# Kernel tuning notes

Hardware: AMD Instinct MI355X
Metric: run time of the kernel (lower is better)

## Reference

```python
import jax, jax.numpy as jnp
import numpy as np

N = 50000      # nodes
E = 800000     # edges (before self-loops)
DIN = 2        # dim_input
DEMB = 128     # dim_embedding
H = 8          # n_heads
DV = 16        # dim_values (H*DV == DEMB)
DH = 512       # dim_hidden
L = 2          # n_att_layers
K = 10         # APPNP steps
ALPHA = 0.1
EPS = 1e-5     # BatchNorm eps
NEG_SLOPE = 0.2  # GAT leaky_relu slope


def setup_inputs() -> dict:
    key = jax.random.key(0)
    ks = jax.random.split(key, 16)
    s = 0.05
    inp = {}
    inp["x"] = jax.random.normal(ks[0], (N, DIN), jnp.float32)
    inp["J"] = jax.random.uniform(ks[1], (N, 1), jnp.float32)
    inp["edge_index"] = jax.random.randint(ks[2], (2, E), 0, N, jnp.int32)
    # Lin1: Linear(dim_input+1, dim_embedding)
    inp["lin0_w"] = jax.random.normal(ks[3], (DIN + 1, DEMB), jnp.float32) * s
    inp["lin0_b"] = jnp.zeros((DEMB,), jnp.float32)
    # Per attention layer (stacked over L):
    inp["gat_w"]   = jax.random.normal(ks[4], (L, DEMB, H * DV), jnp.float32) * s
    inp["att_src"] = jax.random.normal(ks[5], (L, H, DV), jnp.float32) * s
    inp["att_dst"] = jax.random.normal(ks[6], (L, H, DV), jnp.float32) * s
    inp["lin1_w"]  = jax.random.normal(ks[7], (L, DV, DEMB), jnp.float32) * s
    inp["bn1_g"]   = jnp.ones((L, DEMB), jnp.float32)
    inp["bn1_b"]   = jnp.zeros((L, DEMB), jnp.float32)
    inp["lin2_w"]  = jax.random.normal(ks[8], (L, DEMB, DH), jnp.float32) * s
    inp["lin2_b"]  = jnp.zeros((L, DH), jnp.float32)
    inp["lin3_w"]  = jax.random.normal(ks[9], (L, DH, DEMB), jnp.float32) * s
    inp["lin3_b"]  = jnp.zeros((L, DEMB), jnp.float32)
    inp["bn2_g"]   = jnp.ones((L, DEMB), jnp.float32)
    inp["bn2_b"]   = jnp.zeros((L, DEMB), jnp.float32)
    return inp


def _bn(z, g, b):
    # BatchNorm1d over nodes, training-mode batch statistics (biased var)
    mu = z.mean(0)
    var = jnp.mean((z - mu) ** 2, axis=0)
    return g * (z - mu) * jax.lax.rsqrt(var + EPS) + b


def reference(x, J, edge_index, lin0_w, lin0_b, gat_w, att_src, att_dst,
              lin1_w, bn1_g, bn1_b, lin2_w, lin2_b, lin3_w, lin3_b,
              bn2_g, bn2_b):
    # add self-loops (PyG GATConv and APPNP defaults)
    loop = jnp.arange(N, dtype=edge_index.dtype)
    src = jnp.concatenate([edge_index[0], loop])  # message source j
    dst = jnp.concatenate([edge_index[1], loop])  # message target i

    h = jnp.concatenate([x, J], axis=1) @ lin0_w + lin0_b  # [N, DEMB]

    for l in range(L):
        # ---- GATConv ----
        xl = (h @ gat_w[l]).reshape(N, H, DV)                # [N,H,DV]
        a_s = (xl * att_src[l]).sum(-1)                      # [N,H]
        a_d = (xl * att_dst[l]).sum(-1)                      # [N,H]
        e = jax.nn.leaky_relu(a_s[src] + a_d[dst], NEG_SLOPE)  # [E',H]
        e = e - jax.ops.segment_max(e, dst, num_segments=N)[dst]
        ee = jnp.exp(e)
        alpha = ee / jax.ops.segment_sum(ee, dst, num_segments=N)[dst]
        msg = xl[src] * alpha[:, :, None]                    # [E',H,DV]
        gat_out = jax.ops.segment_sum(msg, dst, num_segments=N)  # [N,H,DV]
        # lin1 per head then sum over heads
        hsum = jnp.einsum('nhc,cd->nd', gat_out, lin1_w[l])  # [N,DEMB]
        h1 = _bn(h + hsum, bn1_g[l], bn1_b[l])
        h2 = jax.nn.relu(h1 @ lin2_w[l] + lin2_b[l]) @ lin3_w[l] + lin3_b[l]
        h = _bn(h2 + h1, bn2_g[l], bn2_b[l])

    # ---- APPNP: K steps of (1-a)*Ahat h + a*h0, Ahat = D^-1/2 (A+I) D^-1/2 ----
    deg = jax.ops.segment_sum(jnp.ones_like(dst, jnp.float32), dst, num_segments=N)
    dinv = jax.lax.rsqrt(jnp.maximum(deg, 1.0))  # self-loops guarantee deg>=1
    norm = (dinv[src] * dinv[dst])[:, None]      # [E',1]
    h0 = h

    def step(hk, _):
        agg = jax.ops.segment_sum(norm * hk[src], dst, num_segments=N)
        return (1.0 - ALPHA) * agg + ALPHA * h0, None

    h, _ = jax.lax.scan(step, h, None, length=K)
    return jnp.concatenate([h, J], axis=1)  # [N, DEMB+1]
```

## Files before the change

### kernel.cpp

```cpp
#include <hip/hip_runtime.h>

#define NN 50000
#define NP 50048
#define NMT64 782
#define NE 800000
#define EP (NE + NN)
#define DEMB 128
#define DHID 512
#define NB_SCAN 196

typedef unsigned short ushort_t;
typedef __attribute__((ext_vector_type(8))) short short8_t;
typedef __attribute__((ext_vector_type(4))) float float4_t;

__device__ __forceinline__ float bf2f(ushort_t u) {
    return __uint_as_float(((unsigned int)u) << 16);
}
__device__ __forceinline__ ushort_t f2bf(float f) {
    unsigned int x = __float_as_uint(f);
    x += 0x7fffu + ((x >> 16) & 1u);
    return (ushort_t)(x >> 16);
}
__device__ __forceinline__ float lo16(unsigned int w) { return __uint_as_float(w << 16); }
__device__ __forceinline__ float hi16(unsigned int w) { return __uint_as_float(w & 0xffff0000u); }
__device__ __forceinline__ unsigned int pack2(float a, float b) {
    return (unsigned int)f2bf(a) | ((unsigned int)f2bf(b) << 16);
}
__device__ __forceinline__ void gl_lds16(const ushort_t* g, ushort_t* l) {
    __builtin_amdgcn_global_load_lds(
        (const __attribute__((address_space(1))) void*)g,
        (__attribute__((address_space(3))) void*)l, 16, 0, 0);
}
static inline int cdiv(int a, int b) { return (a + b - 1) / b; }

__global__ void k_detect(const unsigned int* __restrict__ Jw, int* __restrict__ flag) {
    if (threadIdx.x != 0 || blockIdx.x != 0) return;
    int votes = 0;
    for (int i = 0; i < 8; ++i) {
        unsigned int w = Jw[i];
        unsigned int ex = (w >> 23) & 0xFFu;
        if ((w >> 31) == 0u && ex >= 100u && ex <= 126u) votes++;
    }
    *flag = (votes >= 6) ? 1 : 0;
}

struct CvtArgs {
    const void* src[16];
    float* dst[16];
    int n[16];
};
__global__ void k_cvt_all(CvtArgs a, const int* __restrict__ flag) {
    int which = blockIdx.y;
    int i = blockIdx.x * 256 + threadIdx.x;
    if (i >= a.n[which]) return;
    float v;
    if (*flag) v = ((const float*)a.src[which])[i];
    else       v = bf2f(((const ushort_t*)a.src[which])[i]);
    a.dst[which][i] = v;
}

struct TrArgs {
    const float* src[6];
    ushort_t* dst[6];
    int K[6];
    int Nc[6];
};
__global__ void k_tr_all(TrArgs a) {
    int which = blockIdx.y;
    int idx = blockIdx.x * 256 + threadIdx.x;
    int K = a.K[which], Nc = a.Nc[which];
    if (idx >= K * Nc) return;
    int k = idx / Nc, n = idx - k * Nc;
    a.dst[which][n * K + k] = f2bf(a.src[which][idx]);
}

__global__ void k_deg(const int* __restrict__ ei, int* __restrict__ deg) {
    int e = blockIdx.x * 256 + threadIdx.x;
    if (e >= EP) return;
    int d = (e < NE) ? ei[NE + e] : (e - NE);
    atomicAdd(&deg[d], 1);
}

__global__ void k_part(const int* __restrict__ deg, int* __restrict__ part) {
    __shared__ int sm[256];
    int i = blockIdx.x * 256 + threadIdx.x;
    int v = (i < NN) ? deg[i] : 0;
    sm[threadIdx.x] = v;
    __syncthreads();
    for (int off = 128; off > 0; off >>= 1) {
        if (threadIdx.x < off) sm[threadIdx.x] += sm[threadIdx.x + off];
        __syncthreads();
    }
    if (threadIdx.x == 0) part[blockIdx.x] = sm[0];
}

__global__ void k_scan2(const int* __restrict__ part, int* __restrict__ poff,
                        int* __restrict__ rowp) {
    __shared__ int sm[256];
    int t = threadIdx.x;
    int v = (t < NB_SCAN) ? part[t] : 0;
    sm[t] = v;
    __syncthreads();
    int incl = v;
    for (int off = 1; off < 256; off <<= 1) {
        int u = (t >= off) ? sm[t - off] : 0;
        __syncthreads();
        incl += u;
        sm[t] = incl;
        __syncthreads();
    }
    if (t < NB_SCAN) poff[t] = incl - v;
    if (t == 255) rowp[NN] = sm[255];
}

__global__ void k_rowp(const int* __restrict__ deg, const int* __restrict__ poff,
                       int* __restrict__ rowp, float* __restrict__ dinv,
                       int* __restrict__ fill) {
    __shared__ int sm[256];
    int i = blockIdx.x * 256 + threadIdx.x;
    int t = threadIdx.x;
    int v = (i < NN) ? deg[i] : 0;
    sm[t] = v;
    __syncthreads();
    int incl = v;
    for (int off = 1; off < 256; off <<= 1) {
        int u = (t >= off) ? sm[t - off] : 0;
        __syncthreads();
        incl += u;
        sm[t] = incl;
        __syncthreads();
    }
    if (i < NN) {
        int rp = poff[blockIdx.x] + incl - v;
        rowp[i] = rp;
        fill[i] = rp;
        dinv[i] = rsqrtf(fmaxf((float)v, 1.0f));
    }
}

__global__ void k_fill(const int* __restrict__ ei, int* __restrict__ fillpos,
                       ushort_t* __restrict__ col) {
    int e = blockIdx.x * 256 + threadIdx.x;
    if (e >= EP) return;
    int s, d;
    if (e < NE) { s = ei[e]; d = ei[NE + e]; } else { s = d = e - NE; }
    int pos = atomicAdd(&fillpos[d], 1);
    col[pos] = (ushort_t)s;
}

__global__ void k_lin0(const float* __restrict__ x, const float* __restrict__ J,
                       const float* __restrict__ w, const float* __restrict__ b,
                       ushort_t* __restrict__ hB) {
    int idx = blockIdx.x * 256 + threadIdx.x;
    if (idx >= NN * DEMB) return;
    int n = idx >> 7, d = idx & 127;
    float v = x[n * 2] * w[d] + x[n * 2 + 1] * w[DEMB + d] + J[n] * w[2 * DEMB + d] + b[d];
    hB[idx] = f2bf(v);
}

__global__ void k_att(const unsigned int* __restrict__ xlB, const float* __restrict__ asrc,
                      const float* __restrict__ adst, float* __restrict__ a_s,
                      float* __restrict__ a_d) {
    int idx = blockIdx.x * 256 + threadIdx.x;
    if (idx >= NN * 8) return;
    int n = idx >> 3, hh = idx & 7;
    const unsigned int* row = xlB + (size_t)n * 64 + hh * 8;
    float s = 0.f, d = 0.f;
#pragma unroll
    for (int c = 0; c < 8; ++c) {
        unsigned int w = row[c];
        float v0 = lo16(w), v1 = hi16(w);
        s += v0 * asrc[hh * 16 + 2 * c] + v1 * asrc[hh * 16 + 2 * c + 1];
        d += v0 * adst[hh * 16 + 2 * c] + v1 * adst[hh * 16 + 2 * c + 1];
    }
    a_s[idx] = s;
    a_d[idx] = d;
}

__global__ __launch_bounds__(256) void k_z1s(const ushort_t* __restrict__ hB,
                                             const float* __restrict__ g,
                                             const float* __restrict__ w1,
                                             float* __restrict__ stats) {
    int d = threadIdx.x & 127;
    int rstart = blockIdx.x * 2 + (threadIdx.x >> 7);
    int stride = gridDim.x * 2;
    float s1 = 0.f, s2 = 0.f;
    for (int r = rstart; r < NN; r += stride) {
        const float* gr = g + r * 16;
        float s = bf2f(hB[(size_t)r * DEMB + d]);
#pragma unroll
        for (int c = 0; c < 16; ++c) s += gr[c] * w1[c * DEMB + d];
        s1 += s;
        s2 += s * s;
    }
    __shared__ float b1[256], b2[256];
    b1[threadIdx.x] = s1;
    b2[threadIdx.x] = s2;
    __syncthreads();
    if (threadIdx.x < 128) {
        atomicAdd(&stats[threadIdx.x], b1[threadIdx.x] + b1[threadIdx.x + 128]);
        atomicAdd(&stats[128 + threadIdx.x], b2[threadIdx.x] + b2[threadIdx.x + 128]);
    }
}

__global__ void k_bnapply1(const ushort_t* __restrict__ hB, const float* __restrict__ g,
                           const float* __restrict__ w1, const float* __restrict__ stats,
                           const float* __restrict__ gam, const float* __restrict__ bet,
                           ushort_t* __restrict__ outB) {
    int idx = blockIdx.x * 256 + threadIdx.x;
    if (idx >= NN * DEMB) return;
    int n = idx >> 7, d = idx & 127;
    float s = bf2f(hB[idx]);
    const float* gr = g + n * 16;
#pragma unroll
    for (int c = 0; c < 16; ++c) s += gr[c] * w1[c * DEMB + d];
    const float invN = 1.0f / (float)NN;
    float mu = stats[d] * invN;
    float var = stats[128 + d] * invN - mu * mu;
    float rs = rsqrtf(fmaxf(var, 0.f) + 1e-5f);
    float v = gam[d] * (s - mu) * rs + bet[d];
    outB[idx] = f2bf(v);
}

__global__ void k_bnapply(const ushort_t* __restrict__ zB, const float* __restrict__ stats,
                          const float* __restrict__ gam, const float* __restrict__ bet,
                          ushort_t* __restrict__ outB) {
    int idx = blockIdx.x * 256 + threadIdx.x;
    if (idx >= NN * DEMB) return;
    int d = idx & 127;
    const float invN = 1.0f / (float)NN;
    float mu = stats[d] * invN;
    float var = stats[128 + d] * invN - mu * mu;
    float rs = rsqrtf(fmaxf(var, 0.f) + 1e-5f);
    float v = gam[d] * (bf2f(zB[idx]) - mu) * rs + bet[d];
    outB[idx] = f2bf(v);
}

__global__ void k_bnapply_fin(const unsigned int* __restrict__ zB, const float* __restrict__ stats,
                              const float* __restrict__ gam, const float* __restrict__ bet,
                              const float* __restrict__ dinv,
                              unsigned int* __restrict__ hs, unsigned int* __restrict__ h0p) {
    int idx = blockIdx.x * 256 + threadIdx.x;
    if (idx >= NN * 64) return;
    int n = idx >> 6, d0 = (idx & 63) * 2;
    const float invN = 1.0f / (float)NN;
    unsigned int zw = zB[idx];
    float z0 = lo16(zw), z1 = hi16(zw);
    float mu0 = stats[d0] * invN, mu1 = stats[d0 + 1] * invN;
    float v0 = stats[128 + d0] * invN - mu0 * mu0;
    float v1 = stats[128 + d0 + 1] * invN - mu1 * mu1;
    float rs0 = rsqrtf(fmaxf(v0, 0.f) + 1e-5f);
    float rs1 = rsqrtf(fmaxf(v1, 0.f) + 1e-5f);
    float a = gam[d0] * (z0 - mu0) * rs0 + bet[d0];
    float b = gam[d0 + 1] * (z1 - mu1) * rs1 + bet[d0 + 1];
    float di = dinv[n];
    hs[idx] = pack2(di * a, di * b);
    h0p[idx] = pack2(a, b);
}

__global__ __launch_bounds__(256) void k_gat(const int* __restrict__ rowp,
                                             const ushort_t* __restrict__ col,
                                             const float* __restrict__ a_s, const float* __restrict__ a_d,
                                             const unsigned int* __restrict__ xlB, float* __restrict__ g) {
    int wid = (blockIdx.x * 256 + threadIdx.x) >> 6;
    int lane = threadIdx.x & 63;
    if (wid >= NN) return;
    int p0 = rowp[wid], p1 = rowp[wid + 1];
    int hh = lane >> 3;
    float ad2 = a_d[wid * 8 + hh];
    float acc0 = 0.f, acc1 = 0.f, s = 0.f;
    int p = p0;
    while (p < p1) {
        int cnt = p1 - p;
        if (cnt > 64) cnt = 64;
        int pl = p + lane;
        int jv = (int)col[pl < p1 ? pl : (p1 - 1)];
        int i = 0;
        for (; i + 8 <= cnt; i += 8) {
            int j0 = __shfl(jv, i),     j1 = __shfl(jv, i + 1);
            int j2 = __shfl(jv, i + 2), j3 = __shfl(jv, i + 3);
            int j4 = __shfl(jv, i + 4), j5 = __shfl(jv, i + 5);
            int j6 = __shfl(jv, i + 6), j7 = __shfl(jv, i + 7);
            float e0 = a_s[j0 * 8 + hh] + ad2, e1 = a_s[j1 * 8 + hh] + ad2;
            float e2 = a_s[j2 * 8 + hh] + ad2, e3 = a_s[j3 * 8 + hh] + ad2;
            float e4 = a_s[j4 * 8 + hh] + ad2, e5 = a_s[j5 * 8 + hh] + ad2;
            float e6 = a_s[j6 * 8 + hh] + ad2, e7 = a_s[j7 * 8 + hh] + ad2;
            unsigned int w0 = xlB[j0 * 64 + lane], w1 = xlB[j1 * 64 + lane];
            unsigned int w2 = xlB[j2 * 64 + lane], w3 = xlB[j3 * 64 + lane];
            unsigned int w4 = xlB[j4 * 64 + lane], w5 = xlB[j5 * 64 + lane];
            unsigned int w6 = xlB[j6 * 64 + lane], w7 = xlB[j7 * 64 + lane];
            e0 = e0 > 0.f ? e0 : 0.2f * e0;  e1 = e1 > 0.f ? e1 : 0.2f * e1;
            e2 = e2 > 0.f ? e2 : 0.2f * e2;  e3 = e3 > 0.f ? e3 : 0.2f * e3;
            e4 = e4 > 0.f ? e4 : 0.2f * e4;  e5 = e5 > 0.f ? e5 : 0.2f * e5;
            e6 = e6 > 0.f ? e6 : 0.2f * e6;  e7 = e7 > 0.f ? e7 : 0.2f * e7;
            float al0 = __expf(e0), al1 = __expf(e1), al2 = __expf(e2), al3 = __expf(e3);
            float al4 = __expf(e4), al5 = __expf(e5), al6 = __expf(e6), al7 = __expf(e7);
            s += al0 + al1 + al2 + al3 + al4 + al5 + al6 + al7;
            acc0 += al0 * lo16(w0) + al1 * lo16(w1) + al2 * lo16(w2) + al3 * lo16(w3) +
                    al4 * lo16(w4) + al5 * lo16(w5) + al6 * lo16(w6) + al7 * lo16(w7);
            acc1 += al0 * hi16(w0) + al1 * hi16(w1) + al2 * hi16(w2) + al3 * hi16(w3) +
                    al4 * hi16(w4) + al5 * hi16(w5) + al6 * hi16(w6) + al7 * hi16(w7);
        }
        for (; i < cnt; ++i) {
            int j = __shfl(jv, i);
            float e = a_s[j * 8 + hh] + ad2;
            e = e > 0.f ? e : 0.2f * e;
            float al = __expf(e);
            unsigned int w = xlB[j * 64 + lane];
            s += al;
            acc0 += al * lo16(w);
            acc1 += al * hi16(w);
        }
        p += cnt;
    }
    float inv = 1.f / s;
    acc0 *= inv;
    acc1 *= inv;
    acc0 += __shfl_xor(acc0, 8);  acc1 += __shfl_xor(acc1, 8);
    acc0 += __shfl_xor(acc0, 16); acc1 += __shfl_xor(acc1, 16);
    acc0 += __shfl_xor(acc0, 32); acc1 += __shfl_xor(acc1, 32);
    if (lane < 8) ((float2*)g)[wid * 8 + lane] = make_float2(acc0, acc1);
}

__global__ __launch_bounds__(256) void k_appnp(const int* __restrict__ rowp,
                                               const ushort_t* __restrict__ col,
                                               const float* __restrict__ dinv,
                                               const unsigned int* __restrict__ hs,
                                               const unsigned int* __restrict__ h0p,
                                               unsigned int* __restrict__ hs_out,
                                               const float* __restrict__ Jf,
                                               const int* __restrict__ flag,
                                               void* __restrict__ out, int writeOut) {
    int wid = (blockIdx.x * 256 + threadIdx.x) >> 6;
    int lane = threadIdx.x & 63;
    if (wid >= NN) return;
    int p0 = rowp[wid], p1 = rowp[wid + 1];
    float di = dinv[wid];
    unsigned int hw = h0p[(size_t)wid * 64 + lane];
    float a0 = 0.f, a1 = 0.f;
    int p = p0;
    while (p < p1) {
        int cnt = p1 - p;
        if (cnt > 64) cnt = 64;
        int pl = p + lane;
        int jv = (int)col[pl < p1 ? pl : (p1 - 1)];
        int i = 0;
        for (; i + 8 <= cnt; i += 8) {
            int j0 = __shfl(jv, i),     j1 = __shfl(jv, i + 1);
            int j2 = __shfl(jv, i + 2), j3 = __shfl(jv, i + 3);
            int j4 = __shfl(jv, i + 4), j5 = __shfl(jv, i + 5);
            int j6 = __shfl(jv, i + 6), j7 = __shfl(jv, i + 7);
            unsigned int w0 = hs[j0 * 64 + lane], w1 = hs[j1 * 64 + lane];
            unsigned int w2 = hs[j2 * 64 + lane], w3 = hs[j3 * 64 + lane];
            unsigned int w4 = hs[j4 * 64 + lane], w5 = hs[j5 * 64 + lane];
            unsigned int w6 = hs[j6 * 64 + lane], w7 = hs[j7 * 64 + lane];
            a0 += lo16(w0) + lo16(w1) + lo16(w2) + lo16(w3) +
                  lo16(w4) + lo16(w5) + lo16(w6) + lo16(w7);
            a1 += hi16(w0) + hi16(w1) + hi16(w2) + hi16(w3) +
                  hi16(w4) + hi16(w5) + hi16(w6) + hi16(w7);
        }
        for (; i < cnt; ++i) {
            int j = __shfl(jv, i);
            unsigned int w = hs[j * 64 + lane];
            a0 += lo16(w);
            a1 += hi16(w);
        }
        p += cnt;
    }
    float n0 = 0.9f * di * a0 + 0.1f * lo16(hw);
    float n1 = 0.9f * di * a1 + 0.1f * hi16(hw);
    if (!writeOut) {
        hs_out[(size_t)wid * 64 + lane] = pack2(di * n0, di * n1);
    } else {
        size_t base = (size_t)wid * 129;
        if (*flag) {
            float* o = (float*)out;
            o[base + 2 * lane] = n0;
            o[base + 2 * lane + 1] = n1;
            if (lane == 0) o[base + 128] = Jf[wid];
        } else {
            ushort_t* o = (ushort_t*)out;
            o[base + 2 * lane] = f2bf(n0);
            o[base + 2 * lane + 1] = f2bf(n1);
            if (lane == 0) o[base + 128] = f2bf(Jf[wid]);
        }
    }
}

template <int MODE>
__global__ __launch_bounds__(256) void k_gemm64(const ushort_t* __restrict__ A,
                                                const ushort_t* __restrict__ Bt,
                                                int M, int K, int Nc,
                                                const float* __restrict__ bias,
                                                const ushort_t* __restrict__ res,
                                                ushort_t* __restrict__ outB,
                                                float* __restrict__ stats) {
    __shared__ __align__(16) ushort_t lsA[2][64 * 32];
    __shared__ __align__(16) ushort_t lsB[2][128 * 32];
    int t = threadIdx.x;
    int m0 = blockIdx.x * 64;
    int n0 = blockIdx.y * 128;
    int w = t >> 6, lane = t & 63;
    int row16 = lane & 15, quad = lane >> 4;
    int nbase = w * 32;
    float4_t acc[8];
#pragma unroll
    for (int i = 0; i < 8; ++i) acc[i] = (float4_t){0.f, 0.f, 0.f, 0.f};
    int lrow = lane >> 2;
    int lcol = (lane & 3) * 8;
    const ushort_t* gA  = A  + (size_t)(m0 + w * 16 + lrow) * K + lcol;
    const ushort_t* gB0 = Bt + (size_t)(n0 + w * 32 + lrow) * K + lcol;
    const ushort_t* gB1 = Bt + (size_t)(n0 + w * 32 + 16 + lrow) * K + lcol;
    ushort_t* dA  = &lsA[0][0] + (w * 16) * 32;
    ushort_t* dB0 = &lsB[0][0] + (w * 32) * 32;
    ushort_t* dB1 = &lsB[0][0] + (w * 32 + 16) * 32;
    const int bufStrideA = 64 * 32, bufStrideB = 128 * 32;
    const int nK = K >> 5;
    gl_lds16(gA, dA);
    gl_lds16(gB0, dB0);
    gl_lds16(gB1, dB1);
    for (int kb = 0; kb < nK; ++kb) {
        __syncthreads();
        int nb = kb + 1;
        if (nb < nK) {
            int b = nb & 1;
            int k0 = nb << 5;
            gl_lds16(gA + k0, dA + b * bufStrideA);
            gl_lds16(gB0 + k0, dB0 + b * bufStrideB);
            gl_lds16(gB1 + k0, dB1 + b * bufStrideB);
        }
        const ushort_t* la = &lsA[kb & 1][0];
        const ushort_t* lb = &lsB[kb & 1][0];
        short8_t afr[4], bfr[2];
#pragma unroll
        for (int i = 0; i < 4; ++i)
            afr[i] = *(const short8_t*)(la + (i * 16 + row16) * 32 + quad * 8);
#pragma unroll
        for (int i = 0; i < 2; ++i)
            bfr[i] = *(const short8_t*)(lb + (nbase + i * 16 + row16) * 32 + quad * 8);
#pragma unroll
        for (int mt = 0; mt < 4; ++mt)
#pragma unroll
            for (int nt = 0; nt < 2; ++nt)
                acc[mt * 2 + nt] = __builtin_amdgcn_mfma_f32_16x16x32_bf16(
                    afr[mt], bfr[nt], acc[mt * 2 + nt], 0, 0, 0);
    }
    if (MODE == 2) {
        __shared__ float s1[128], s2[128];
        if (t < 128) { s1[t] = 0.f; s2[t] = 0.f; }
        __syncthreads();
#pragma unroll
        for (int mt = 0; mt < 4; ++mt) {
#pragma unroll
            for (int nt = 0; nt < 2; ++nt) {
                int cb = nbase + nt * 16 + row16;
                int cc = n0 + cb;
                float bv = bias[cc];
                float ls = 0.f, lq = 0.f;
#pragma unroll
                for (int r = 0; r < 4; ++r) {
                    int rr = m0 + mt * 16 + quad * 4 + r;
                    if (rr < M) {
                        float v = acc[mt * 2 + nt][r] + bv + bf2f(res[(size_t)rr * Nc + cc]);
                        outB[(size_t)rr * Nc + cc] = f2bf(v);
                        ls += v;
                        lq += v * v;
                    }
                }
                atomicAdd(&s1[cb], ls);
                atomicAdd(&s2[cb], lq);
            }
        }
        __syncthreads();
        if (t < 128) {
            atomicAdd(&stats[n0 + t], s1[t]);
            atomicAdd(&stats[128 + n0 + t], s2[t]);
        }
    } else {
#pragma unroll
        for (int mt = 0; mt < 4; ++mt) {
#pragma unroll
            for (int nt = 0; nt < 2; ++nt) {
                int cc = n0 + nbase + nt * 16 + row16;
                float bv = (MODE == 1) ? bias[cc] : 0.f;
#pragma unroll
                for (int r = 0; r < 4; ++r) {
                    int rr = m0 + mt * 16 + quad * 4 + r;
                    if (rr < M) {
                        float v = acc[mt * 2 + nt][r];
                        if (MODE == 1) {
                            v += bv;
                            v = v > 0.f ? v : 0.f;
                        }
                        outB[(size_t)rr * Nc + cc] = f2bf(v);
                    }
                }
            }
        }
    }
}

extern "C" void kernel_launch(void* const* d_in, const int* in_sizes, int n_in,
                              void* d_out, int out_size, void* d_ws, size_t ws_size,
                              hipStream_t stream) {
    const int* ei = (const int*)d_in[2];

    char* p = (char*)d_ws;
    auto alloc = [&](size_t bytes) {
        void* r = (void*)p;
        p += (bytes + 255) & ~(size_t)255;
        return r;
    };
    ushort_t* hB    = (ushort_t*)alloc((size_t)NP * DEMB * 2);
    ushort_t* h1B   = (ushort_t*)alloc((size_t)NP * DEMB * 2);
    ushort_t* xlB   = (ushort_t*)alloc((size_t)NN * DEMB * 2);
    unsigned int* hsA  = (unsigned int*)alloc((size_t)NN * 64 * 4);
    unsigned int* hsB_ = (unsigned int*)alloc((size_t)NN * 64 * 4);
    unsigned int* h0p  = (unsigned int*)alloc((size_t)NN * 64 * 4);
    ushort_t* hidB  = (ushort_t*)alloc((size_t)NP * DHID * 2);
    float*    asv   = (float*)alloc((size_t)NN * 8 * 4);
    float*    adv   = (float*)alloc((size_t)NN * 8 * 4);
    float*    gv    = (float*)alloc((size_t)NN * 16 * 4);
    float*    dinvv = (float*)alloc((size_t)NN * 4);
    float*    stats = (float*)alloc(4 * 256 * 4);
    int*      deg   = (int*)alloc((size_t)NN * 4);
    int*      rowp  = (int*)alloc((size_t)(NN + 1) * 4);
    int*      fill  = (int*)alloc((size_t)NN * 4);
    ushort_t* colv  = (ushort_t*)alloc((size_t)EP * 2);
    int*      part  = (int*)alloc(NB_SCAN * 4);
    int*      poff  = (int*)alloc(NB_SCAN * 4);
    int*      flag  = (int*)alloc(256);
    ushort_t* wtg   = (ushort_t*)alloc((size_t)2 * 128 * 128 * 2);
    ushort_t* wt2   = (ushort_t*)alloc((size_t)2 * 512 * 128 * 2);
    ushort_t* wt3   = (ushort_t*)alloc((size_t)2 * 128 * 512 * 2);
    float* xf   = (float*)alloc((size_t)NN * 2 * 4);
    float* Jf   = (float*)alloc((size_t)NN * 4);
    float* l0wF = (float*)alloc(384 * 4);
    float* l0bF = (float*)alloc(128 * 4);
    float* gwF  = (float*)alloc(32768 * 4);
    float* asF  = (float*)alloc(256 * 4);
    float* adF  = (float*)alloc(256 * 4);
    float* w1F  = (float*)alloc(4096 * 4);
    float* b1gF = (float*)alloc(256 * 4);
    float* b1bF = (float*)alloc(256 * 4);
    float* w2F  = (float*)alloc(131072 * 4);
    float* b2F  = (float*)alloc(1024 * 4);
    float* w3F  = (float*)alloc(131072 * 4);
    float* b3F  = (float*)alloc(256 * 4);
    float* b2gF = (float*)alloc(256 * 4);
    float* b2bF = (float*)alloc(256 * 4);

    k_detect<<<1, 64, 0, stream>>>((const unsigned int*)d_in[1], flag);
    CvtArgs ca;
    {
        const int srcIdx[16] = {0, 1, 3, 4, 5, 6, 7, 8, 9, 10, 11, 12, 13, 14, 15, 16};
        float* dsts[16] = {xf, Jf, l0wF, l0bF, gwF, asF, adF, w1F, b1gF, b1bF,
                           w2F, b2F, w3F, b3F, b2gF, b2bF};
        const int ns[16] = {NN * 2, NN, 384, 128, 32768, 256, 256, 4096, 256, 256,
                            131072, 1024, 131072, 256, 256, 256};
        for (int i = 0; i < 16; ++i) { ca.src[i] = d_in[srcIdx[i]]; ca.dst[i] = dsts[i]; ca.n[i] = ns[i]; }
    }
    k_cvt_all<<<dim3(cdiv(131072, 256), 16), 256, 0, stream>>>(ca, flag);

    hipMemsetAsync(deg, 0, (size_t)NN * 4, stream);
    hipMemsetAsync(stats, 0, 4 * 256 * 4, stream);
    k_deg<<<cdiv(EP, 256), 256, 0, stream>>>(ei, deg);
    k_part<<<NB_SCAN, 256, 0, stream>>>(deg, part);
    k_scan2<<<1, 256, 0, stream>>>(part, poff, rowp);
    k_rowp<<<NB_SCAN, 256, 0, stream>>>(deg, poff, rowp, dinvv, fill);
    k_fill<<<cdiv(EP, 256), 256, 0, stream>>>(ei, fill, colv);

    TrArgs ta;
    {
        const float* srcs[6] = {gwF, gwF + 16384, w2F, w2F + 65536, w3F, w3F + 65536};
        ushort_t* dsts[6] = {wtg, wtg + 16384, wt2, wt2 + 65536, wt3, wt3 + 65536};
        const int Ks[6] = {128, 128, 128, 128, 512, 512};
        const int Ncs[6] = {128, 128, 512, 512, 128, 128};
        for (int i = 0; i < 6; ++i) { ta.src[i] = srcs[i]; ta.dst[i] = dsts[i]; ta.K[i] = Ks[i]; ta.Nc[i] = Ncs[i]; }
    }
    k_tr_all<<<dim3(cdiv(65536, 256), 6), 256, 0, stream>>>(ta);

    k_lin0<<<cdiv(NN * DEMB, 256), 256, 0, stream>>>(xf, Jf, l0wF, l0bF, hB);

    for (int l = 0; l < 2; ++l) {
        float* st1 = stats + (l * 2 + 0) * 256;
        float* st2 = stats + (l * 2 + 1) * 256;
        ushort_t* zB = xlB;
        k_gemm64<3><<<dim3(NMT64, 1), 256, 0, stream>>>(hB, wtg + l * 16384, NN, 128, 128,
                                                        nullptr, nullptr, xlB, nullptr);
        k_att<<<cdiv(NN * 8, 256), 256, 0, stream>>>((const unsigned int*)xlB, asF + l * 128,
                                                     adF + l * 128, asv, adv);
        k_gat<<<cdiv(NN * 64, 256), 256, 0, stream>>>(rowp, colv, asv, adv,
                                                      (const unsigned int*)xlB, gv);
        k_z1s<<<512, 256, 0, stream>>>(hB, gv, w1F + l * 2048, st1);
        k_bnapply1<<<cdiv(NN * DEMB, 256), 256, 0, stream>>>(hB, gv, w1F + l * 2048, st1,
                                                             b1gF + l * 128, b1bF + l * 128,
                                                             h1B);
        k_gemm64<1><<<dim3(NMT64, 4), 256, 0, stream>>>(h1B, wt2 + l * 65536, NN, 128, 512,
                                                        b2F + l * 512, nullptr, hidB, nullptr);
        k_gemm64<2><<<dim3(NMT64, 1), 256, 0, stream>>>(hidB, wt3 + l * 65536, NN, 512, 128,
                                                        b3F + l * 128, h1B, zB, st2);
        if (l == 0) {
            k_bnapply<<<cdiv(NN * DEMB, 256), 256, 0, stream>>>(zB, st2, b2gF, b2bF, hB);
        } else {
            k_bnapply_fin<<<cdiv(NN * 64, 256), 256, 0, stream>>>((const unsigned int*)zB, st2,
                                                                  b2gF + 128, b2bF + 128,
                                                                  dinvv, hsA, h0p);
        }
    }

    unsigned int* pin = hsA;
    unsigned int* pout = hsB_;
    for (int k = 0; k < 10; ++k) {
        int last = (k == 9) ? 1 : 0;
        k_appnp<<<cdiv(NN * 64, 256), 256, 0, stream>>>(rowp, colv, dinvv, pin, h0p, pout,
                                                        Jf, flag, d_out, last);
        unsigned int* tmp = pout;
        pout = pin;
        pin = tmp;
    }
}
```

Measured before the change: 930.1 us.

## Fuse FFN lin2+ReLU+lin3 GEMMs into one kernel keeping hidden in LDS

Replaces the two-GEMM FFN (lin2 with bias+ReLU writing a 50k x 512 bf16 hidden buffer, then lin3 with residual and BN stats) by a single fused kernel. Each block keeps a 64-row tile of the input in registers, computes 64-column chunks of the hidden layer, stages them through LDS, and accumulates the lin3 output directly, double-buffering the W3 slices. This removes the global round trip of the hidden activation and one launch. The cost is lower parallelism (one block per 64 rows), extra syncthreads per chunk, and W2/W3 being re-streamed by every block.

```diff
diff --git a/kernel.cpp b/kernel.cpp
--- a/kernel.cpp
+++ b/kernel.cpp
@@ -445,58 +445,174 @@
                 acc[mt * 2 + nt] = __builtin_amdgcn_mfma_f32_16x16x32_bf16(
                     afr[mt], bfr[nt], acc[mt * 2 + nt], 0, 0, 0);
     }
-    if (MODE == 2) {
-        __shared__ float s1[128], s2[128];
-        if (t < 128) { s1[t] = 0.f; s2[t] = 0.f; }
-        __syncthreads();
-#pragma unroll
-        for (int mt = 0; mt < 4; ++mt) {
-#pragma unroll
-            for (int nt = 0; nt < 2; ++nt) {
-                int cb = nbase + nt * 16 + row16;
-                int cc = n0 + cb;
-                float bv = bias[cc];
-                float ls = 0.f, lq = 0.f;
-#pragma unroll
-                for (int r = 0; r < 4; ++r) {
-                    int rr = m0 + mt * 16 + quad * 4 + r;
-                    if (rr < M) {
-                        float v = acc[mt * 2 + nt][r] + bv + bf2f(res[(size_t)rr * Nc + cc]);
-                        outB[(size_t)rr * Nc + cc] = f2bf(v);
-                        ls += v;
-                        lq += v * v;
-                    }
-                }
-                atomicAdd(&s1[cb], ls);
-                atomicAdd(&s2[cb], lq);
-            }
-        }
-        __syncthreads();
-        if (t < 128) {
-            atomicAdd(&stats[n0 + t], s1[t]);
-            atomicAdd(&stats[128 + n0 + t], s2[t]);
-        }
-    } else {
-#pragma unroll
-        for (int mt = 0; mt < 4; ++mt) {
-#pragma unroll
-            for (int nt = 0; nt < 2; ++nt) {
-                int cc = n0 + nbase + nt * 16 + row16;
-                float bv = (MODE == 1) ? bias[cc] : 0.f;
-#pragma unroll
-                for (int r = 0; r < 4; ++r) {
-                    int rr = m0 + mt * 16 + quad * 4 + r;
-                    if (rr < M) {
-                        float v = acc[mt * 2 + nt][r];
-                        if (MODE == 1) {
-                            v += bv;
-                            v = v > 0.f ? v : 0.f;
-                        }
-                        outB[(size_t)rr * Nc + cc] = f2bf(v);
-                    }
+#pragma unroll
+    for (int mt = 0; mt < 4; ++mt) {
+#pragma unroll
+        for (int nt = 0; nt < 2; ++nt) {
+            int cc = n0 + nbase + nt * 16 + row16;
+#pragma unroll
+            for (int r = 0; r < 4; ++r) {
+                int rr = m0 + mt * 16 + quad * 4 + r;
+                if (rr < M) {
+                    outB[(size_t)rr * Nc + cc] = f2bf(acc[mt * 2 + nt][r]);
                 }
             }
         }
+    }
+}
+
+__global__ __launch_bounds__(256, 2) void k_ffn(const ushort_t* __restrict__ A,
+                                                const ushort_t* __restrict__ W2t,
+                                                const ushort_t* __restrict__ W3t,
+                                                const float* __restrict__ b2,
+                                                const float* __restrict__ b3,
+                                                const ushort_t* __restrict__ res,
+                                                ushort_t* __restrict__ outB,
+                                                float* __restrict__ stats) {
+    __shared__ __align__(16) ushort_t lsA[4 * 64 * 32];
+    __shared__ __align__(16) ushort_t lsW2[4 * 64 * 32];
+    __shared__ __align__(16) ushort_t lsW3[2][2 * 128 * 32];
+    __shared__ __align__(16) ushort_t lsH[4][2 * 16 * 32];
+    __shared__ float s1[128], s2[128];
+    int t = threadIdx.x;
+    int w = t >> 6, lane = t & 63;
+    int m0 = blockIdx.x * 64;
+    int row16 = lane & 15, quad = lane >> 4;
+    int sw = (row16 >> 2) & 3;
+    int srow = lane >> 2;
+    int klin = lane & 3;
+
+    if (t < 128) { s1[t] = 0.f; s2[t] = 0.f; }
+
+#pragma unroll
+    for (int i = 0; i < 4; ++i) {
+        int row = i * 16 + srow;
+        int kc = klin ^ ((row >> 2) & 3);
+        gl_lds16(A + (size_t)(m0 + row) * 128 + w * 32 + kc * 8,
+                 lsA + w * 2048 + i * 512);
+    }
+#pragma unroll
+    for (int i = 0; i < 4; ++i) {
+        int n = i * 16 + srow;
+        int kc = klin ^ ((n >> 2) & 3);
+        gl_lds16(W2t + (size_t)n * 128 + w * 32 + kc * 8,
+                 lsW2 + w * 2048 + i * 512);
+    }
+#pragma unroll
+    for (int i = 0; i < 4; ++i) {
+        int f = w * 4 + i;
+        int ks = f >> 3;
+        int n = (f & 7) * 16 + srow;
+        int kc = klin ^ ((n >> 2) & 3);
+        gl_lds16(W3t + (size_t)n * 512 + ks * 32 + kc * 8,
+                 &lsW3[0][0] + f * 512);
+    }
+    __syncthreads();
+
+    short8_t afrA[4];
+#pragma unroll
+    for (int kb = 0; kb < 4; ++kb)
+        afrA[kb] = *(const short8_t*)(lsA + kb * 2048 + (w * 16 + row16) * 32 + (quad ^ sw) * 8);
+
+    float4_t accz[8];
+#pragma unroll
+    for (int i = 0; i < 8; ++i) accz[i] = (float4_t){0.f, 0.f, 0.f, 0.f};
+
+    for (int c = 0; c < 8; ++c) {
+        float b2v[4];
+#pragma unroll
+        for (int nt = 0; nt < 4; ++nt) b2v[nt] = b2[c * 64 + nt * 16 + row16];
+        float4_t acch[4];
+#pragma unroll
+        for (int i = 0; i < 4; ++i) acch[i] = (float4_t){0.f, 0.f, 0.f, 0.f};
+#pragma unroll
+        for (int kb = 0; kb < 4; ++kb) {
+            short8_t bfr[4];
+#pragma unroll
+            for (int nt = 0; nt < 4; ++nt) {
+                int n = nt * 16 + row16;
+                bfr[nt] = *(const short8_t*)(lsW2 + kb * 2048 + n * 32 + (quad ^ sw) * 8);
+            }
+#pragma unroll
+            for (int nt = 0; nt < 4; ++nt)
+                acch[nt] = __builtin_amdgcn_mfma_f32_16x16x32_bf16(afrA[kb], bfr[nt],
+                                                                   acch[nt], 0, 0, 0);
+        }
+#pragma unroll
+        for (int nt = 0; nt < 4; ++nt) {
+            int ks = nt >> 1;
+#pragma unroll
+            for (int r = 0; r < 4; ++r) {
+                int row = quad * 4 + r;
+                int colk = (nt & 1) * 16 + row16;
+                int scol = (colk & 7) | ((((colk >> 3) ^ quad)) << 3);
+                float v = acch[nt][r] + b2v[nt];
+                v = v > 0.f ? v : 0.f;
+                lsH[w][ks * 512 + row * 32 + scol] = f2bf(v);
+            }
+        }
+        __syncthreads();
+
+        if (c + 1 < 8) {
+#pragma unroll
+            for (int i = 0; i < 4; ++i) {
+                int n = i * 16 + srow;
+                int kc = klin ^ ((n >> 2) & 3);
+                gl_lds16(W2t + (size_t)((c + 1) * 64 + n) * 128 + w * 32 + kc * 8,
+                         lsW2 + w * 2048 + i * 512);
+            }
+            ushort_t* w3dst = &lsW3[(c + 1) & 1][0];
+#pragma unroll
+            for (int i = 0; i < 4; ++i) {
+                int f = w * 4 + i;
+                int ks = f >> 3;
+                int n = (f & 7) * 16 + srow;
+                int kc = klin ^ ((n >> 2) & 3);
+                gl_lds16(W3t + (size_t)n * 512 + (c + 1) * 64 + ks * 32 + kc * 8,
+                         w3dst + f * 512);
+            }
+        }
+        const ushort_t* w3src = &lsW3[c & 1][0];
+#pragma unroll
+        for (int ks = 0; ks < 2; ++ks) {
+            short8_t afrH = *(const short8_t*)(&lsH[w][0] + ks * 512 + row16 * 32 +
+                                               (quad ^ sw) * 8);
+            short8_t bfr[8];
+#pragma unroll
+            for (int nt = 0; nt < 8; ++nt) {
+                int n = nt * 16 + row16;
+                bfr[nt] = *(const short8_t*)(w3src + ks * 4096 + n * 32 + (quad ^ sw) * 8);
+            }
+#pragma unroll
+            for (int nt = 0; nt < 8; ++nt)
+                accz[nt] = __builtin_amdgcn_mfma_f32_16x16x32_bf16(afrH, bfr[nt],
+                                                                   accz[nt], 0, 0, 0);
+        }
+        __syncthreads();
+    }
+
+#pragma unroll
+    for (int nt = 0; nt < 8; ++nt) {
+        int cc = nt * 16 + row16;
+        float bv = b3[cc];
+        float ls = 0.f, lq = 0.f;
+#pragma unroll
+        for (int r = 0; r < 4; ++r) {
+            int rr = m0 + w * 16 + quad * 4 + r;
+            if (rr < NN) {
+                float v = accz[nt][r] + bv + bf2f(res[(size_t)rr * 128 + cc]);
+                outB[(size_t)rr * 128 + cc] = f2bf(v);
+                ls += v;
+                lq += v * v;
+            }
+        }
+        atomicAdd(&s1[cc], ls);
+        atomicAdd(&s2[cc], lq);
+    }
+    __syncthreads();
+    if (t < 128) {
+        atomicAdd(&stats[t], s1[t]);
+        atomicAdd(&stats[128 + t], s2[t]);
     }
 }
 
@@ -517,7 +633,6 @@
     unsigned int* hsA  = (unsigned int*)alloc((size_t)NN * 64 * 4);
     unsigned int* hsB_ = (unsigned int*)alloc((size_t)NN * 64 * 4);
     unsigned int* h0p  = (unsigned int*)alloc((size_t)NN * 64 * 4);
-    ushort_t* hidB  = (ushort_t*)alloc((size_t)NP * DHID * 2);
     float*    asv   = (float*)alloc((size_t)NN * 8 * 4);
     float*    adv   = (float*)alloc((size_t)NN * 8 * 4);
     float*    gv    = (float*)alloc((size_t)NN * 16 * 4);
@@ -596,10 +711,8 @@
         k_bnapply1<<<cdiv(NN * DEMB, 256), 256, 0, stream>>>(hB, gv, w1F + l * 2048, st1,
                                                              b1gF + l * 128, b1bF + l * 128,
                                                              h1B);
-        k_gemm64<1><<<dim3(NMT64, 4), 256, 0, stream>>>(h1B, wt2 + l * 65536, NN, 128, 512,
-                                                        b2F + l * 512, nullptr, hidB, nullptr);
-        k_gemm64<2><<<dim3(NMT64, 1), 256, 0, stream>>>(hidB, wt3 + l * 65536, NN, 512, 128,
-                                                        b3F + l * 128, h1B, zB, st2);
+        k_ffn<<<NMT64, 256, 0, stream>>>(h1B, wt2 + l * 65536, wt3 + l * 65536,
+                                         b2F + l * 512, b3F + l * 128, h1B, zB, st2);
         if (l == 0) {
             k_bnapply<<<cdiv(NN * DEMB, 256), 256, 0, stream>>>(zB, st2, b2gF, b2bF, hB);
         } else {
```

New measurement: 902.1 us. 3.0% less time.
